# Optimization experiments

Hardware: AMD Instinct MI355X
Metric: run time of the kernel (lower is better)

The kernel has to match this reference:

```python
import jax, jax.numpy as jnp
import numpy as np

HEADS = 16
DIM_HEAD = 64
SOFTCAP = 50.0
ROPE_THETA = 10000.0


def setup_inputs() -> dict:
    key = jax.random.key(0)
    ks = jax.random.split(key, 5)
    b, n, d, m, lmax = 2, 2048, 1024, 4, 256
    x = jax.random.normal(ks[0], (b, n, d), dtype=jnp.float32)
    tokens = jax.random.normal(ks[1], (b, m, lmax, d), dtype=jnp.float32)
    offsets = jnp.array([100, 600, 1100, 1600], dtype=jnp.int64)
    modalities = jnp.stack(
        [jnp.zeros_like(offsets), offsets, jnp.full_like(offsets, lmax)], axis=-1
    )  # [m, 3] = (type, offset, length)
    modalities = jnp.broadcast_to(modalities, (b, m, 3))
    gamma = jax.random.normal(ks[2], (d,), dtype=jnp.float32) * 0.02
    w_qkv = jax.random.normal(ks[3], (d, 3 * HEADS * DIM_HEAD), dtype=jnp.float32) / np.sqrt(d)
    w_out = jax.random.normal(ks[4], (HEADS * DIM_HEAD, d), dtype=jnp.float32) / np.sqrt(d)
    return {"x": x, "tokens": tokens, "gamma": gamma, "w_qkv": w_qkv,
            "w_out": w_out, "modalities": modalities}


def _apply_rotary(t, pos):
    # t: [b h n dh], pos: [b n] integer rotary positions (interleaved-pair rotation)
    freqs = 1.0 / (ROPE_THETA ** (jnp.arange(0, DIM_HEAD, 2, dtype=jnp.float32) / DIM_HEAD))
    ang = pos[:, None, :, None].astype(jnp.float32) * freqs  # [b 1 n dh/2]
    cos, sin = jnp.cos(ang), jnp.sin(ang)
    t1, t2 = t[..., ::2], t[..., 1::2]
    out = jnp.stack([t1 * cos - t2 * sin, t1 * sin + t2 * cos], axis=-1)
    return out.reshape(t.shape)


def reference(x, tokens, gamma, w_qkv, w_out, modalities):
    b, n, d = x.shape
    lmax = tokens.shape[2]
    off = modalities[..., 1]   # [b m]
    ln = modalities[..., 2]    # [b m]
    seq = jnp.arange(n)

    # --- embed_modality_tokens: scatter modality tokens into sequence ---
    in_span = (seq[None, None, :] >= off[..., None]) & (seq[None, None, :] < (off + ln)[..., None])  # [b m n]
    is_any = in_span.any(axis=1)  # [b n]
    rel = jnp.clip(seq[None, None, :] - off[..., None], 0, lmax - 1)  # [b m n]
    gathered = jnp.take_along_axis(tokens, rel[..., None], axis=2)  # [b m n d]
    mod_embed = jnp.einsum('bmn,bmnd->bnd', in_span.astype(x.dtype), gathered)
    x = jnp.where(is_any[..., None], mod_embed, x)

    # --- derive_rotary_positions_from_modality_positions (offset=[+1,-1]) ---
    rot_span = (seq[None, None, :] >= (off + 1)[..., None]) & (seq[None, None, :] < (off + ln)[..., None])
    pos = seq[None, :] - jnp.cumsum(rot_span.any(axis=1).astype(jnp.int32), axis=-1)  # [b n]

    # --- naive_attn_mask: causal OR within-modality bidirectional ---
    causal = seq[:, None] >= seq[None, :]  # [i j]
    mod_mask = ((seq[None, None, :, None] >= off[..., None, None]) &
                (seq[None, None, None, :] < (off + ln)[..., None, None])).any(axis=1)  # [b i j]
    mask = causal[None] | mod_mask  # [b i j]

    # --- Attention ---
    scale = DIM_HEAD ** -0.5
    xn = x / jnp.clip(jnp.linalg.norm(x, axis=-1, keepdims=True), 1e-12)
    xn = xn * (d ** 0.5) * (gamma + 1.0)  # RMSNorm (l2norm * sqrt(dim) * (gamma+1))
    qkv = (xn @ w_qkv).reshape(b, n, 3, HEADS, DIM_HEAD)
    q, k, v = (jnp.transpose(qkv[:, :, i], (0, 2, 1, 3)) for i in range(3))  # [b h n dh]
    q = _apply_rotary(q, pos)
    k = _apply_rotary(k, pos)
    scores = jnp.einsum('bhid,bhjd->bhij', q, k) * scale
    scores = jnp.tanh(scores / SOFTCAP) * SOFTCAP  # softclamp
    scores = jnp.where(mask[:, None], scores, -jnp.inf)
    attn = jax.nn.softmax(scores, axis=-1)
    out = jnp.einsum('bhij,bhjd->bhid', attn, v)
    out = jnp.transpose(out, (0, 2, 1, 3)).reshape(b, n, HEADS * DIM_HEAD)
    return out @ w_out
```

## Files before the change

kernel.cpp:

```cpp
#include <hip/hip_runtime.h>
#include <stdint.h>

#define HH 16
#define DHD 64
#define BB 2
#define NN 2048
#define DD 1024
#define MMOD 4
#define LMAX 256
#define BNROWS (BB*NN)
#define QKVN (3*HH*DHD)

typedef __attribute__((ext_vector_type(4))) float f32x4;
typedef __attribute__((ext_vector_type(8))) short s16x8;
typedef __attribute__((ext_vector_type(4))) short s16x4;

__device__ __forceinline__ float bf2f(unsigned short b) {
  return __uint_as_float(((unsigned int)b) << 16);
}
__device__ __forceinline__ unsigned short f2bf(float f) {
  unsigned int u = __float_as_uint(f);
  u += 0x7fffu + ((u >> 16) & 1u);
  return (unsigned short)(u >> 16);
}
__device__ __forceinline__ unsigned int cvt_pk_bf16(float a, float b) {
  unsigned int r;
  asm("v_cvt_pk_bf16_f32 %0, %1, %2" : "=v"(r) : "v"(a), "v"(b));
  return r;
}

#define ASYNC_LDS16(g, l) \
  __builtin_amdgcn_global_load_lds((const __attribute__((address_space(1))) void*)(g), \
                                   (__attribute__((address_space(3))) void*)(l), 16, 0, 0)

__global__ __launch_bounds__(256) void k_prep(const float* __restrict__ x,
                                              const float* __restrict__ tokens,
                                              const float* __restrict__ gamma,
                                              const int* __restrict__ mods,
                                              unsigned short* __restrict__ xn) {
  int bs = blockIdx.x;
  int bb = bs / NN, s = bs % NN;
  int t = threadIdx.x;
  int c = t * 4;
  const float4 xv = *(const float4*)(x + (size_t)bs * DD + c);
  float4 acc = {0.f, 0.f, 0.f, 0.f};
  bool any = false;
  #pragma unroll
  for (int m = 0; m < MMOD; ++m) {
    int off = mods[(bb * MMOD + m) * 3 + 1];
    int ln  = mods[(bb * MMOD + m) * 3 + 2];
    if (s >= off && s < off + ln) {
      any = true;
      int rel = s - off;
      if (rel > LMAX - 1) rel = LMAX - 1;
      if (rel < 0) rel = 0;
      const float4 tv = *(const float4*)(tokens + ((size_t)(bb * MMOD + m) * LMAX + rel) * DD + c);
      acc.x += tv.x; acc.y += tv.y; acc.z += tv.z; acc.w += tv.w;
    }
  }
  float4 v = any ? acc : xv;
  float ss = v.x*v.x + v.y*v.y + v.z*v.z + v.w*v.w;
  #pragma unroll
  for (int o = 32; o; o >>= 1) ss += __shfl_xor(ss, o);
  __shared__ float red[4];
  int wv = t >> 6;
  if ((t & 63) == 0) red[wv] = ss;
  __syncthreads();
  float tot = red[0] + red[1] + red[2] + red[3];
  float norm = sqrtf(tot);
  norm = fmaxf(norm, 1e-12f);
  float sc = 32.0f / norm;
  const float4 g = *(const float4*)(gamma + c);
  unsigned long long pk =
      (unsigned long long)f2bf(v.x * sc * (g.x + 1.f)) |
      ((unsigned long long)f2bf(v.y * sc * (g.y + 1.f)) << 16) |
      ((unsigned long long)f2bf(v.z * sc * (g.z + 1.f)) << 32) |
      ((unsigned long long)f2bf(v.w * sc * (g.w + 1.f)) << 48);
  *(unsigned long long*)(xn + (size_t)bs * DD + c) = pk;
}

__global__ void k_pos(const int* __restrict__ mods, int* __restrict__ pos) {
  int bb = blockIdx.x;
  int lane = threadIdx.x;
  int offs[MMOD], ends[MMOD];
  #pragma unroll
  for (int m = 0; m < MMOD; ++m) {
    int off = mods[(bb * MMOD + m) * 3 + 1];
    int ln  = mods[(bb * MMOD + m) * 3 + 2];
    offs[m] = off + 1;
    ends[m] = off + ln;
  }
  int base = lane * (NN / 64);
  int lc[NN / 64];
  int tot = 0;
  #pragma unroll
  for (int i = 0; i < NN / 64; ++i) {
    int s = base + i;
    int f = 0;
    #pragma unroll
    for (int m = 0; m < MMOD; ++m)
      if (s >= offs[m] && s < ends[m]) f = 1;
    tot += f;
    lc[i] = tot;
  }
  int v = tot;
  #pragma unroll
  for (int o = 1; o < 64; o <<= 1) {
    int u = __shfl_up(v, o);
    if (lane >= o) v += u;
  }
  int excl = v - tot;
  #pragma unroll
  for (int i = 0; i < NN / 64; ++i)
    pos[bb * NN + base + i] = base + i - (excl + lc[i]);
}

__global__ void k_tab(const int* __restrict__ pos, float2* __restrict__ tab) {
  int gid = blockIdx.x * 256 + threadIdx.x;
  int p = gid & 31;
  int bs = gid >> 5;
  float inv = expf(-((float)p / 32.f) * 9.210340371976184f);
  float ang = (float)pos[bs] * inv;
  float sn, cs;
  sincosf(ang, &sn, &cs);
  tab[gid] = make_float2(cs, sn);
}

__global__ void k_tr(const float* __restrict__ in, unsigned short* __restrict__ out,
                     int R, int C) {
  __shared__ float tile[32][33];
  int bx = blockIdx.x, by = blockIdx.y;
  int tx = threadIdx.x, ty = threadIdx.y;
  #pragma unroll
  for (int k = 0; k < 4; ++k) {
    int r = by * 32 + ty + k * 8, c = bx * 32 + tx;
    tile[ty + k * 8][tx] = in[(size_t)r * C + c];
  }
  __syncthreads();
  #pragma unroll
  for (int k = 0; k < 4; ++k) {
    int oc = bx * 32 + ty + k * 8;
    int orr = by * 32 + tx;
    out[(size_t)oc * R + orr] = f2bf(tile[tx][ty + k * 8]);
  }
}

template<bool F32OUT>
__global__ __launch_bounds__(256) void k_gemm(const unsigned short* __restrict__ A,
                                              const unsigned short* __restrict__ Bt,
                                              void* __restrict__ Cp,
                                              int M, int Nn, int K) {
  __shared__ unsigned short As[2][128 * 64];
  __shared__ unsigned short Bs[2][128 * 64];
  int tid = threadIdx.x;
  int lane = tid & 63, wv = tid >> 6;
  int lo = lane & 15, hi = lane >> 4;
  int nb = gridDim.x * gridDim.y;
  int fid = blockIdx.y * gridDim.x + blockIdx.x;
  int cpx = nb >> 3;
  int nid = (fid & 7) * cpx + (fid >> 3);
  int m0 = (nid / gridDim.x) * 128;
  int n0 = (nid % gridDim.x) * 128;
  int wr = wv >> 1, wc = wv & 1;
  f32x4 acc[4][4] = {};

  int srow = tid >> 3;
  int scs  = ((tid & 7) ^ ((tid >> 3) & 7)) * 8;
  #define STAGE_G(BUF, KT) do { \
    _Pragma("unroll") \
    for (int is_ = 0; is_ < 4; ++is_) { \
      int r_ = is_ * 32 + srow; \
      const unsigned short* ga_ = A  + (size_t)(m0 + r_) * K + (KT) + scs; \
      const unsigned short* gb_ = Bt + (size_t)(n0 + r_) * K + (KT) + scs; \
      ASYNC_LDS16(ga_, &As[BUF][(is_ * 256 + wv * 64) * 8]); \
      ASYNC_LDS16(gb_, &Bs[BUF][(is_ * 256 + wv * 64) * 8]); \
    } \
  } while (0)

  int nt = K >> 6;
  STAGE_G(0, 0);
  __syncthreads();
  int buf = 0;
  for (int t = 0; t < nt; ++t) {
    if (t + 1 < nt) STAGE_G(buf ^ 1, (t + 1) << 6);
    #pragma unroll
    for (int ks = 0; ks < 2; ++ks) {
      s16x8 af[4], bfr[4];
      #pragma unroll
      for (int m = 0; m < 4; ++m) {
        int row = wr * 64 + m * 16 + lo;
        int cc = ((ks * 4 + hi) ^ (lo & 7)) * 8;
        af[m] = *(const s16x8*)&As[buf][row * 64 + cc];
      }
      #pragma unroll
      for (int nn = 0; nn < 4; ++nn) {
        int row = wc * 64 + nn * 16 + lo;
        int cc = ((ks * 4 + hi) ^ (lo & 7)) * 8;
        bfr[nn] = *(const s16x8*)&Bs[buf][row * 64 + cc];
      }
      #pragma unroll
      for (int m = 0; m < 4; ++m)
        #pragma unroll
        for (int nn = 0; nn < 4; ++nn)
          acc[m][nn] = __builtin_amdgcn_mfma_f32_16x16x32_bf16(af[m], bfr[nn], acc[m][nn], 0, 0, 0);
    }
    __syncthreads();
    buf ^= 1;
  }
  #undef STAGE_G

  #pragma unroll
  for (int m = 0; m < 4; ++m) {
    #pragma unroll
    for (int nn = 0; nn < 4; ++nn) {
      int r0 = m0 + wr * 64 + m * 16 + hi * 4;
      int cc = n0 + wc * 64 + nn * 16 + lo;
      #pragma unroll
      for (int j = 0; j < 4; ++j) {
        float val = acc[m][nn][j];
        if (F32OUT) ((float*)Cp)[(size_t)(r0 + j) * Nn + cc] = val;
        else        ((unsigned short*)Cp)[(size_t)(r0 + j) * Nn + cc] = f2bf(val);
      }
    }
  }
}

template<bool F32OUT>
__global__ __launch_bounds__(256) void k_gemm_n64(const unsigned short* __restrict__ A,
                                                  const unsigned short* __restrict__ Bt,
                                                  void* __restrict__ Cp,
                                                  int M, int Nn, int K) {
  __shared__ unsigned short As[2][128 * 64];
  __shared__ unsigned short Bs[2][64 * 64];
  int tid = threadIdx.x;
  int lane = tid & 63, wv = tid >> 6;
  int lo = lane & 15, hi = lane >> 4;
  int nb = gridDim.x * gridDim.y;
  int fid = blockIdx.y * gridDim.x + blockIdx.x;
  int cpx = nb >> 3;
  int nid = (fid & 7) * cpx + (fid >> 3);
  int m0 = (nid / gridDim.x) * 128;
  int n0 = (nid % gridDim.x) * 64;
  f32x4 acc[2][4] = {};

  int srow = tid >> 3;
  int scs  = ((tid & 7) ^ ((tid >> 3) & 7)) * 8;
  #define STAGE_N(BUF, KT) do { \
    _Pragma("unroll") \
    for (int is_ = 0; is_ < 4; ++is_) { \
      int r_ = is_ * 32 + srow; \
      const unsigned short* ga_ = A + (size_t)(m0 + r_) * K + (KT) + scs; \
      ASYNC_LDS16(ga_, &As[BUF][(is_ * 256 + wv * 64) * 8]); \
    } \
    _Pragma("unroll") \
    for (int is_ = 0; is_ < 2; ++is_) { \
      int r_ = is_ * 32 + srow; \
      const unsigned short* gb_ = Bt + (size_t)(n0 + r_) * K + (KT) + scs; \
      ASYNC_LDS16(gb_, &Bs[BUF][(is_ * 256 + wv * 64) * 8]); \
    } \
  } while (0)

  int nt = K >> 6;
  STAGE_N(0, 0);
  __syncthreads();
  int buf = 0;
  for (int t = 0; t < nt; ++t) {
    if (t + 1 < nt) STAGE_N(buf ^ 1, (t + 1) << 6);
    #pragma unroll
    for (int ks = 0; ks < 2; ++ks) {
      s16x8 af[2], bfr[4];
      #pragma unroll
      for (int m = 0; m < 2; ++m) {
        int row = wv * 32 + m * 16 + lo;
        int cc = ((ks * 4 + hi) ^ (lo & 7)) * 8;
        af[m] = *(const s16x8*)&As[buf][row * 64 + cc];
      }
      #pragma unroll
      for (int nn = 0; nn < 4; ++nn) {
        int row = nn * 16 + lo;
        int cc = ((ks * 4 + hi) ^ (lo & 7)) * 8;
        bfr[nn] = *(const s16x8*)&Bs[buf][row * 64 + cc];
      }
      #pragma unroll
      for (int m = 0; m < 2; ++m)
        #pragma unroll
        for (int nn = 0; nn < 4; ++nn)
          acc[m][nn] = __builtin_amdgcn_mfma_f32_16x16x32_bf16(af[m], bfr[nn], acc[m][nn], 0, 0, 0);
    }
    __syncthreads();
    buf ^= 1;
  }
  #undef STAGE_N

  #pragma unroll
  for (int m = 0; m < 2; ++m)
    #pragma unroll
    for (int nn = 0; nn < 4; ++nn) {
      int r0 = m0 + wv * 32 + m * 16 + hi * 4;
      int cc = n0 + nn * 16 + lo;
      #pragma unroll
      for (int j = 0; j < 4; ++j) {
        float val = acc[m][nn][j];
        if (F32OUT) ((float*)Cp)[(size_t)(r0 + j) * Nn + cc] = val;
        else        ((unsigned short*)Cp)[(size_t)(r0 + j) * Nn + cc] = f2bf(val);
      }
    }
}

__global__ __launch_bounds__(256) void k_rope(const unsigned short* __restrict__ qkv,
                                              const float2* __restrict__ tab,
                                              unsigned short* __restrict__ k) {
  int bs = blockIdx.x;
  int bb = bs / NN, s = bs % NN;
  int lane = threadIdx.x & 63, wv = threadIdx.x >> 6;
  #pragma unroll
  for (int g = 16 + wv; g < 32; g += 4) {
    int h = g & 15;
    float val = bf2f(qkv[(size_t)bs * QKVN + g * 64 + lane]);
    float partner = __shfl_xor(val, 1);
    float2 cs = tab[(size_t)bs * 32 + (lane >> 1)];
    float out;
    if ((lane & 1) == 0) out = val * cs.x - partner * cs.y;
    else                 out = partner * cs.y + val * cs.x;
    k[((size_t)(bb * HH + h) * NN + s) * 64 + lane] = f2bf(out);
  }
}

__global__ __launch_bounds__(256) void k_vtr(const unsigned short* __restrict__ qkvt,
                                             unsigned short* __restrict__ vT) {
  __shared__ unsigned short t[64][72];
  int s0 = blockIdx.x * 64, bh = blockIdx.y, bb = bh >> 4, h = bh & 15;
  int tid = threadIdx.x;
  int r = tid >> 2, c0 = (tid & 3) * 16;
  int cw = c0 ^ (((r >> 4) & 3) << 4);
  const unsigned short* src = qkvt + (size_t)(bb * NN + s0 + r) * QKVN + 2048 + h * 64 + c0;
  *(s16x8*)&t[r][cw]     = *(const s16x8*)src;
  *(s16x8*)&t[r][cw + 8] = *(const s16x8*)(src + 8);
  __syncthreads();
  int dh = tid >> 2, sc = (tid & 3) * 16;
  int col2 = dh ^ ((tid & 3) << 4);
  s16x8 o1, o2;
  #pragma unroll
  for (int i = 0; i < 8; ++i) {
    o1[i] = (short)t[sc + i][col2];
    o2[i] = (short)t[sc + 8 + i][col2];
  }
  unsigned short* dst = vT + ((size_t)bh * 64 + dh) * NN + s0;
  int pb = (sc & 32) + (((sc >> 4) & 1) << 2);
  s16x4 g0 = __builtin_shufflevector(o1, o1, 0, 1, 2, 3);
  s16x4 g1 = __builtin_shufflevector(o1, o1, 4, 5, 6, 7);
  s16x4 g2 = __builtin_shufflevector(o2, o2, 0, 1, 2, 3);
  s16x4 g3 = __builtin_shufflevector(o2, o2, 4, 5, 6, 7);
  *(s16x4*)&dst[pb]      = g0;
  *(s16x4*)&dst[pb + 8]  = g1;
  *(s16x4*)&dst[pb + 16] = g2;
  *(s16x4*)&dst[pb + 24] = g3;
}

__global__ __launch_bounds__(512) void k_attn(const unsigned short* __restrict__ qkvt,
                                              const float2* __restrict__ tab,
                                              const unsigned short* __restrict__ k,
                                              const unsigned short* __restrict__ vT,
                                              const int* __restrict__ mods,
                                              unsigned short* __restrict__ o) {
  __shared__ unsigned short Ks[2][128 * 64];
  __shared__ unsigned short Vs[2][64 * 128];
  int tid = threadIdx.x;
  int lane = tid & 63, wv = tid >> 6;
  int lo = lane & 15, hi = lane >> 4;

  int fid = blockIdx.y * gridDim.x + blockIdx.x;
  int nid = (fid & 7) * 64 + (fid >> 3);
  int bh = nid >> 4;
  int bx = nid & 15;
  int bb = bh >> 4;
  int h = bh & 15;
  int q0A = (31 - bx) * 64;
  int q0B = bx * 64;
  int q0w = ((wv < 4) ? q0A : q0B) + (wv & 3) * 16;

  const unsigned short* kb = k + (size_t)bh * NN * 64;
  const unsigned short* vb = vT + (size_t)bh * 64 * NN;

  s16x8 qf[2];
  {
    int qrow = q0w + lo;
    const unsigned short* qp = qkvt + (size_t)(bb * NN + qrow) * QKVN + h * 64;
    const float2* tb = tab + (size_t)(bb * NN + qrow) * 32;
    #pragma unroll
    for (int ks = 0; ks < 2; ++ks) {
      s16x8 raw = *(const s16x8*)&qp[ks * 32 + hi * 8];
      #pragma unroll
      for (int e2 = 0; e2 < 4; ++e2) {
        float2 cs = tb[ks * 16 + hi * 4 + e2];
        float t1 = bf2f((unsigned short)raw[2 * e2]);
        float t2 = bf2f((unsigned short)raw[2 * e2 + 1]);
        float o1 = (t1 * cs.x - t2 * cs.y) * 0.18033688011112042f;
        float o2 = (t1 * cs.y + t2 * cs.x) * 0.18033688011112042f;
        qf[ks][2 * e2]     = (short)f2bf(o1);
        qf[ks][2 * e2 + 1] = (short)f2bf(o2);
      }
    }
  }

  int off_[MMOD], end_[MMOD];
  #pragma unroll
  for (int m = 0; m < MMOD; ++m) {
    off_[m] = mods[(bb * MMOD + m) * 3 + 1];
    end_[m] = off_[m] + mods[(bb * MMOD + m) * 3 + 2];
  }
  int limit_l;
  {
    int r = q0w + lo;
    int L = r + 1;
    #pragma unroll
    for (int m = 0; m < MMOD; ++m)
      if (off_[m] <= r && end_[m] > L) L = end_[m];
    limit_l = L;
  }
  int minlim, kvmax_w;
  {
    int L = q0w + 1;
    #pragma unroll
    for (int m = 0; m < MMOD; ++m)
      if (off_[m] <= q0w && end_[m] > L) L = end_[m];
    minlim = L;
    int r = q0w + 15;
    int L2 = r + 1;
    #pragma unroll
    for (int m = 0; m < MMOD; ++m)
      if (off_[m] <= r && end_[m] > L2) L2 = end_[m];
    kvmax_w = L2;
  }
  int nt;
  {
    int ra = q0A + 63;
    int LA = ra + 1;
    #pragma unroll
    for (int m = 0; m < MMOD; ++m)
      if (off_[m] <= ra && end_[m] > LA) LA = end_[m];
    int rb2 = q0B + 63;
    int LB = rb2 + 1;
    #pragma unroll
    for (int m = 0; m < MMOD; ++m)
      if (off_[m] <= rb2 && end_[m] > LB) LB = end_[m];
    int Lblk = (LA > LB) ? LA : LB;
    nt = (Lblk + 127) >> 7;
  }

  #define STAGE_KV(B, KV0) do { \
    _Pragma("unroll") \
    for (int i_ = 0; i_ < 2; ++i_) { \
      int rK_ = i_ * 64 + (tid >> 3); \
      int csK_ = (lane & 7) ^ ((tid >> 3) & 7); \
      const unsigned short* gK_ = kb + (size_t)((KV0) + rK_) * 64 + csK_ * 8; \
      ASYNC_LDS16(gK_, &Ks[B][(i_ * 512 + wv * 64) * 8]); \
      int dhV_ = i_ * 32 + wv * 4 + (lane >> 4); \
      int ccV_ = ((lane & 7) ^ (dhV_ & 7)) | (lane & 8); \
      const unsigned short* gV_ = vb + (size_t)dhV_ * NN + (KV0) + ccV_ * 8; \
      ASYNC_LDS16(gV_, &Vs[B][(i_ * 512 + wv * 64) * 8]); \
    } \
  } while (0)

  float lr = 0.f;
  f32x4 accO[4] = {};

  STAGE_KV(0, 0);
  __syncthreads();
  int buf = 0;
  for (int t = 0; t < nt; ++t) {
    if (t + 1 < nt) STAGE_KV(buf ^ 1, (t + 1) << 7);
    int kv0 = t << 7;
    if (kv0 < kvmax_w) {
      f32x4 sv[8];
      __builtin_amdgcn_s_setprio(1);
      #pragma unroll
      for (int cb = 0; cb < 8; ++cb) {
        int krow = cb * 16 + lo;
        int c0 = (hi) ^ (krow & 7);
        int c1 = (4 + hi) ^ (krow & 7);
        s16x8 kf0 = *(const s16x8*)&Ks[buf][krow * 64 + c0 * 8];
        s16x8 kf1 = *(const s16x8*)&Ks[buf][krow * 64 + c1 * 8];
        f32x4 z = {};
        z = __builtin_amdgcn_mfma_f32_16x16x32_bf16(kf0, qf[0], z, 0, 0, 0);
        z = __builtin_amdgcn_mfma_f32_16x16x32_bf16(kf1, qf[1], z, 0, 0, 0);
        sv[cb] = z;
      }
      __builtin_amdgcn_s_setprio(0);

      unsigned int pk_[8][2];
      bool edge = (kv0 + 128 > minlim);
      int kb0 = kv0 + hi * 4;
      #pragma unroll
      for (int cb = 0; cb < 8; ++cb) {
        float p[4];
        #pragma unroll
        for (int j = 0; j < 4; ++j) {
          float s = sv[cb][j];
          float u = __builtin_fmaf(s * s, -6.40604e-5f, 1.0f);
          float pp = __builtin_amdgcn_exp2f(s * u);
          if (edge && (kb0 + cb * 16 + j) >= limit_l) pp = 0.f;
          p[j] = pp;
        }
        lr += (p[0] + p[1]) + (p[2] + p[3]);
        pk_[cb][0] = cvt_pk_bf16(p[0], p[1]);
        pk_[cb][1] = cvt_pk_bf16(p[2], p[3]);
      }

      union { unsigned int u[4]; s16x8 v; } pa[4];
      #pragma unroll
      for (int kk = 0; kk < 4; ++kk) {
        pa[kk].u[0] = pk_[2 * kk][0];
        pa[kk].u[1] = pk_[2 * kk][1];
        pa[kk].u[2] = pk_[2 * kk + 1][0];
        pa[kk].u[3] = pk_[2 * kk + 1][1];
      }

      __builtin_amdgcn_s_setprio(1);
      #pragma unroll
      for (int ks = 0; ks < 4; ++ks) {
        #pragma unroll
        for (int cbo = 0; cbo < 4; ++cbo) {
          int vrow = cbo * 16 + lo;
          int vc = (ks * 4 + hi) ^ (vrow & 7);
          s16x8 vf = *(const s16x8*)&Vs[buf][vrow * 128 + vc * 8];
          accO[cbo] = __builtin_amdgcn_mfma_f32_16x16x32_bf16(pa[ks].v, vf, accO[cbo], 0, 0, 0);
        }
      }
      __builtin_amdgcn_s_setprio(0);
    }
    __syncthreads();
    buf ^= 1;
  }

  lr += __shfl_xor(lr, 16);
  lr += __shfl_xor(lr, 32);
  float rl[4];
  #pragma unroll
  for (int j = 0; j < 4; ++j)
    rl[j] = __builtin_amdgcn_rcpf(__shfl(lr, hi * 4 + j));

  #pragma unroll
  for (int cb = 0; cb < 4; ++cb)
    #pragma unroll
    for (int j = 0; j < 4; ++j) {
      int r = q0w + hi * 4 + j;
      float val = accO[cb][j] * rl[j];
      o[((size_t)(bb * NN) + r) * (HH * DHD) + h * 64 + cb * 16 + lo] = f2bf(val);
    }
}

extern "C" void kernel_launch(void* const* d_in, const int* in_sizes, int n_in,
                              void* d_out, int out_size, void* d_ws, size_t ws_size,
                              hipStream_t stream) {
  (void)in_sizes; (void)n_in; (void)out_size; (void)ws_size;
  const float* x      = (const float*)d_in[0];
  const float* tokens = (const float*)d_in[1];
  const float* gamma  = (const float*)d_in[2];
  const float* w_qkv  = (const float*)d_in[3];
  const float* w_out  = (const float*)d_in[4];
  const int*   mods   = (const int*)d_in[5];

  char* ws = (char*)d_ws;
  unsigned short* xn    = (unsigned short*)(ws + 0);
  unsigned short* wqkvT = (unsigned short*)(ws + 8388608);
  unsigned short* woutT = (unsigned short*)(ws + 14680064);
  unsigned short* qkvt  = (unsigned short*)(ws + 16777216);
  unsigned short* kd    = (unsigned short*)(ws + 50331648);
  unsigned short* vTd   = (unsigned short*)(ws + 58720256);
  unsigned short* attno = (unsigned short*)(ws + 67108864);
  int*            pos   = (int*)(ws + 75497472);
  float2*         tab   = (float2*)(ws + 75513856);

  k_prep<<<BNROWS, 256, 0, stream>>>(x, tokens, gamma, mods, xn);
  k_pos<<<BB, 64, 0, stream>>>(mods, pos);
  k_tab<<<(BB * NN * 32) / 256, 256, 0, stream>>>(pos, tab);
  k_tr<<<dim3(QKVN / 32, DD / 32), dim3(32, 8), 0, stream>>>(w_qkv, wqkvT, DD, QKVN);
  k_tr<<<dim3((HH * DHD) / 32, DD / 32), dim3(32, 8), 0, stream>>>(w_out, woutT, HH * DHD, DD);
  k_gemm<false><<<dim3(QKVN / 128, BNROWS / 128), 256, 0, stream>>>(xn, wqkvT, (void*)qkvt, BNROWS, QKVN, DD);
  k_rope<<<BNROWS, 256, 0, stream>>>(qkvt, tab, kd);
  k_vtr<<<dim3(NN / 64, BB * HH), 256, 0, stream>>>(qkvt, vTd);
  k_attn<<<dim3(16, BB * HH), 512, 0, stream>>>(qkvt, tab, kd, vTd, mods, attno);
  k_gemm_n64<true><<<dim3(DD / 64, BNROWS / 128), 256, 0, stream>>>(attno, woutT, (void*)d_out, BNROWS, DD, HH * DHD);
}
```

Baseline: 134.5 us.

## Split KV tile across wave pairs with 32-row Q per wave in attention

Each wave now handles 32 query rows (two 16-row fragments) and half of each 128-key tile. Each K and V fragment read from LDS feeds two MFMAs, which raises reuse and cuts LDS traffic per FLOP. The two half-tile partial accumulators and row sums are combined through shared memory at the end, and launch bounds now request 4 blocks. The cost is more accumulator registers, an extra LDS reduction with a barrier, and only half the waves writing output.

```diff
diff --git a/kernel.cpp b/kernel.cpp
--- a/kernel.cpp
+++ b/kernel.cpp
@@ -357,17 +357,20 @@
   *(s16x4*)&dst[pb + 24] = g3;
 }
 
-__global__ __launch_bounds__(512) void k_attn(const unsigned short* __restrict__ qkvt,
-                                              const float2* __restrict__ tab,
-                                              const unsigned short* __restrict__ k,
-                                              const unsigned short* __restrict__ vT,
-                                              const int* __restrict__ mods,
-                                              unsigned short* __restrict__ o) {
+__global__ __launch_bounds__(512, 4) void k_attn(const unsigned short* __restrict__ qkvt,
+                                                 const float2* __restrict__ tab,
+                                                 const unsigned short* __restrict__ k,
+                                                 const unsigned short* __restrict__ vT,
+                                                 const int* __restrict__ mods,
+                                                 unsigned short* __restrict__ o) {
   __shared__ unsigned short Ks[2][128 * 64];
   __shared__ unsigned short Vs[2][64 * 128];
   int tid = threadIdx.x;
   int lane = tid & 63, wv = tid >> 6;
   int lo = lane & 15, hi = lane >> 4;
+  int t_ = wv >> 2;
+  int rg = (wv >> 1) & 1;
+  int hf = wv & 1;
 
   int fid = blockIdx.y * gridDim.x + blockIdx.x;
   int nid = (fid & 7) * 64 + (fid >> 3);
@@ -377,14 +380,15 @@
   int h = bh & 15;
   int q0A = (31 - bx) * 64;
   int q0B = bx * 64;
-  int q0w = ((wv < 4) ? q0A : q0B) + (wv & 3) * 16;
+  int q0w = (t_ ? q0B : q0A) + rg * 32;
 
   const unsigned short* kb = k + (size_t)bh * NN * 64;
   const unsigned short* vb = vT + (size_t)bh * 64 * NN;
 
-  s16x8 qf[2];
-  {
-    int qrow = q0w + lo;
+  s16x8 qf[2][2];
+  #pragma unroll
+  for (int fr = 0; fr < 2; ++fr) {
+    int qrow = q0w + fr * 16 + lo;
     const unsigned short* qp = qkvt + (size_t)(bb * NN + qrow) * QKVN + h * 64;
     const float2* tb = tab + (size_t)(bb * NN + qrow) * 32;
     #pragma unroll
@@ -397,8 +401,8 @@
         float t2 = bf2f((unsigned short)raw[2 * e2 + 1]);
         float o1 = (t1 * cs.x - t2 * cs.y) * 0.18033688011112042f;
         float o2 = (t1 * cs.y + t2 * cs.x) * 0.18033688011112042f;
-        qf[ks][2 * e2]     = (short)f2bf(o1);
-        qf[ks][2 * e2 + 1] = (short)f2bf(o2);
+        qf[fr][ks][2 * e2]     = (short)f2bf(o1);
+        qf[fr][ks][2 * e2 + 1] = (short)f2bf(o2);
       }
     }
   }
@@ -409,14 +413,15 @@
     off_[m] = mods[(bb * MMOD + m) * 3 + 1];
     end_[m] = off_[m] + mods[(bb * MMOD + m) * 3 + 2];
   }
-  int limit_l;
-  {
-    int r = q0w + lo;
+  int limit_lf[2];
+  #pragma unroll
+  for (int fr = 0; fr < 2; ++fr) {
+    int r = q0w + fr * 16 + lo;
     int L = r + 1;
     #pragma unroll
     for (int m = 0; m < MMOD; ++m)
       if (off_[m] <= r && end_[m] > L) L = end_[m];
-    limit_l = L;
+    limit_lf[fr] = L;
   }
   int minlim, kvmax_w;
   {
@@ -425,7 +430,7 @@
     for (int m = 0; m < MMOD; ++m)
       if (off_[m] <= q0w && end_[m] > L) L = end_[m];
     minlim = L;
-    int r = q0w + 15;
+    int r = q0w + 31;
     int L2 = r + 1;
     #pragma unroll
     for (int m = 0; m < MMOD; ++m)
@@ -462,69 +467,77 @@
     } \
   } while (0)
 
-  float lr = 0.f;
-  f32x4 accO[4] = {};
+  float lrf[2] = {0.f, 0.f};
+  f32x4 accO[2][4] = {};
 
   STAGE_KV(0, 0);
   __syncthreads();
   int buf = 0;
   for (int t = 0; t < nt; ++t) {
     if (t + 1 < nt) STAGE_KV(buf ^ 1, (t + 1) << 7);
-    int kv0 = t << 7;
-    if (kv0 < kvmax_w) {
-      f32x4 sv[8];
+    int kv0h = (t << 7) + hf * 64;
+    if (kv0h < kvmax_w) {
+      f32x4 sv[2][4];
       __builtin_amdgcn_s_setprio(1);
       #pragma unroll
-      for (int cb = 0; cb < 8; ++cb) {
-        int krow = cb * 16 + lo;
+      for (int cb = 0; cb < 4; ++cb) {
+        int krow = hf * 64 + cb * 16 + lo;
         int c0 = (hi) ^ (krow & 7);
         int c1 = (4 + hi) ^ (krow & 7);
         s16x8 kf0 = *(const s16x8*)&Ks[buf][krow * 64 + c0 * 8];
         s16x8 kf1 = *(const s16x8*)&Ks[buf][krow * 64 + c1 * 8];
-        f32x4 z = {};
-        z = __builtin_amdgcn_mfma_f32_16x16x32_bf16(kf0, qf[0], z, 0, 0, 0);
-        z = __builtin_amdgcn_mfma_f32_16x16x32_bf16(kf1, qf[1], z, 0, 0, 0);
-        sv[cb] = z;
+        #pragma unroll
+        for (int fr = 0; fr < 2; ++fr) {
+          f32x4 z = {};
+          z = __builtin_amdgcn_mfma_f32_16x16x32_bf16(kf0, qf[fr][0], z, 0, 0, 0);
+          z = __builtin_amdgcn_mfma_f32_16x16x32_bf16(kf1, qf[fr][1], z, 0, 0, 0);
+          sv[fr][cb] = z;
+        }
       }
       __builtin_amdgcn_s_setprio(0);
 
-      unsigned int pk_[8][2];
-      bool edge = (kv0 + 128 > minlim);
-      int kb0 = kv0 + hi * 4;
-      #pragma unroll
-      for (int cb = 0; cb < 8; ++cb) {
-        float p[4];
-        #pragma unroll
-        for (int j = 0; j < 4; ++j) {
-          float s = sv[cb][j];
-          float u = __builtin_fmaf(s * s, -6.40604e-5f, 1.0f);
-          float pp = __builtin_amdgcn_exp2f(s * u);
-          if (edge && (kb0 + cb * 16 + j) >= limit_l) pp = 0.f;
-          p[j] = pp;
+      unsigned int pk_[2][4][2];
+      bool edge = (kv0h + 64 > minlim);
+      int kb0 = kv0h + hi * 4;
+      #pragma unroll
+      for (int fr = 0; fr < 2; ++fr)
+        #pragma unroll
+        for (int cb = 0; cb < 4; ++cb) {
+          float p[4];
+          #pragma unroll
+          for (int j = 0; j < 4; ++j) {
+            float s = sv[fr][cb][j];
+            float u = __builtin_fmaf(s * s, -6.40604e-5f, 1.0f);
+            float pp = __builtin_amdgcn_exp2f(s * u);
+            if (edge && (kb0 + cb * 16 + j) >= limit_lf[fr]) pp = 0.f;
+            p[j] = pp;
+          }
+          lrf[fr] += (p[0] + p[1]) + (p[2] + p[3]);
+          pk_[fr][cb][0] = cvt_pk_bf16(p[0], p[1]);
+          pk_[fr][cb][1] = cvt_pk_bf16(p[2], p[3]);
         }
-        lr += (p[0] + p[1]) + (p[2] + p[3]);
-        pk_[cb][0] = cvt_pk_bf16(p[0], p[1]);
-        pk_[cb][1] = cvt_pk_bf16(p[2], p[3]);
-      }
-
-      union { unsigned int u[4]; s16x8 v; } pa[4];
-      #pragma unroll
-      for (int kk = 0; kk < 4; ++kk) {
-        pa[kk].u[0] = pk_[2 * kk][0];
-        pa[kk].u[1] = pk_[2 * kk][1];
-        pa[kk].u[2] = pk_[2 * kk + 1][0];
-        pa[kk].u[3] = pk_[2 * kk + 1][1];
-      }
+
+      union { unsigned int u[4]; s16x8 v; } pa[2][2];
+      #pragma unroll
+      for (int fr = 0; fr < 2; ++fr)
+        #pragma unroll
+        for (int ks2 = 0; ks2 < 2; ++ks2) {
+          pa[fr][ks2].u[0] = pk_[fr][2 * ks2][0];
+          pa[fr][ks2].u[1] = pk_[fr][2 * ks2][1];
+          pa[fr][ks2].u[2] = pk_[fr][2 * ks2 + 1][0];
+          pa[fr][ks2].u[3] = pk_[fr][2 * ks2 + 1][1];
+        }
 
       __builtin_amdgcn_s_setprio(1);
       #pragma unroll
-      for (int ks = 0; ks < 4; ++ks) {
+      for (int ks2 = 0; ks2 < 2; ++ks2) {
         #pragma unroll
         for (int cbo = 0; cbo < 4; ++cbo) {
           int vrow = cbo * 16 + lo;
-          int vc = (ks * 4 + hi) ^ (vrow & 7);
+          int vc = ((hf * 2 + ks2) * 4 + hi) ^ (vrow & 7);
           s16x8 vf = *(const s16x8*)&Vs[buf][vrow * 128 + vc * 8];
-          accO[cbo] = __builtin_amdgcn_mfma_f32_16x16x32_bf16(pa[ks].v, vf, accO[cbo], 0, 0, 0);
+          accO[0][cbo] = __builtin_amdgcn_mfma_f32_16x16x32_bf16(pa[0][ks2].v, vf, accO[0][cbo], 0, 0, 0);
+          accO[1][cbo] = __builtin_amdgcn_mfma_f32_16x16x32_bf16(pa[1][ks2].v, vf, accO[1][cbo], 0, 0, 0);
         }
       }
       __builtin_amdgcn_s_setprio(0);
@@ -533,21 +546,48 @@
     buf ^= 1;
   }
 
-  lr += __shfl_xor(lr, 16);
-  lr += __shfl_xor(lr, 32);
-  float rl[4];
-  #pragma unroll
-  for (int j = 0; j < 4; ++j)
-    rl[j] = __builtin_amdgcn_rcpf(__shfl(lr, hi * 4 + j));
-
-  #pragma unroll
-  for (int cb = 0; cb < 4; ++cb)
-    #pragma unroll
-    for (int j = 0; j < 4; ++j) {
-      int r = q0w + hi * 4 + j;
-      float val = accO[cb][j] * rl[j];
-      o[((size_t)(bb * NN) + r) * (HH * DHD) + h * 64 + cb * 16 + lo] = f2bf(val);
-    }
+  #pragma unroll
+  for (int fr = 0; fr < 2; ++fr) {
+    lrf[fr] += __shfl_xor(lrf[fr], 16);
+    lrf[fr] += __shfl_xor(lrf[fr], 32);
+  }
+
+  float* accbuf = (float*)&Ks[0][0];
+  float* lrbuf  = (float*)&Vs[0][0];
+  if (lane < 16) {
+    lrbuf[wv * 32 + lo]      = lrf[0];
+    lrbuf[wv * 32 + 16 + lo] = lrf[1];
+  }
+  if (hf == 1) {
+    float* ab = accbuf + ((size_t)(wv >> 1) * 64 + lane) * 32;
+    #pragma unroll
+    for (int fr = 0; fr < 2; ++fr)
+      #pragma unroll
+      for (int cbo = 0; cbo < 4; ++cbo)
+        #pragma unroll
+        for (int j = 0; j < 4; ++j)
+          ab[fr * 16 + cbo * 4 + j] = accO[fr][cbo][j];
+  }
+  __syncthreads();
+  if (hf == 0) {
+    const float* ab = accbuf + ((size_t)(wv >> 1) * 64 + lane) * 32;
+    #pragma unroll
+    for (int fr = 0; fr < 2; ++fr) {
+      #pragma unroll
+      for (int j = 0; j < 4; ++j) {
+        int row32 = fr * 16 + hi * 4 + j;
+        float lt = lrbuf[wv * 32 + row32] + lrbuf[(wv + 1) * 32 + row32];
+        float rl = __builtin_amdgcn_rcpf(lt);
+        int rout = q0w + row32;
+        size_t base = ((size_t)(bb * NN) + rout) * (HH * DHD) + h * 64;
+        #pragma unroll
+        for (int cbo = 0; cbo < 4; ++cbo) {
+          float val = (accO[fr][cbo][j] + ab[fr * 16 + cbo * 4 + j]) * rl;
+          o[base + cbo * 16 + lo] = f2bf(val);
+        }
+      }
+    }
+  }
 }
 
 extern "C" void kernel_launch(void* const* d_in, const int* in_sizes, int n_in,
```

Result: slower. 142.4 us (+5.8%).
